# Optimization experiments

Measured on AMD Instinct MI355X. Metric: run time of the kernel, lower is better.

## Reference

```python
import jax, jax.numpy as jnp
import numpy as np

B, H, W, C = 64, 56, 56, 128
WIN, SHIFT, NH = 7, 3, 4
HD = C // NH
N = WIN * WIN
HID = 4 * C
EPS = 1e-5


def _rel_index():
    coords = np.stack(np.meshgrid(np.arange(WIN), np.arange(WIN), indexing='ij')).reshape(2, -1)
    rel = coords[:, :, None] - coords[:, None, :]
    rel = rel.transpose(1, 2, 0).astype(np.int64)
    rel[..., 0] += WIN - 1
    rel[..., 1] += WIN - 1
    rel[..., 0] *= 2 * WIN - 1
    return rel.sum(-1)  # [N, N]


def _attn_mask():
    img = np.zeros((H, W), dtype=np.float32)
    cnt = 0
    bounds = [(0, H - WIN), (H - WIN, H - SHIFT), (H - SHIFT, H)]
    for h0, h1 in bounds:
        for w0, w1 in bounds:
            img[h0:h1, w0:w1] = cnt
            cnt += 1
    mw = img.reshape(H // WIN, WIN, W // WIN, WIN).transpose(0, 2, 1, 3).reshape(-1, N)
    am = mw[:, None, :] - mw[:, :, None]
    return np.where(am != 0, -100.0, 0.0).astype(np.float32)  # [nW, N, N]


def setup_inputs() -> dict:
    key = jax.random.key(0)
    ks = jax.random.split(key, 16)
    s = lambda k, shp, f: (jax.random.normal(k, shp, jnp.float32) * f)
    return {
        'x': s(ks[0], (B, H * W, C), 1.0),
        'norm1_w': jnp.ones((C,), jnp.float32),
        'norm1_b': jnp.zeros((C,), jnp.float32),
        'qkv_w': s(ks[1], (3 * C, C), 0.02),
        'qkv_b': jnp.zeros((3 * C,), jnp.float32),
        'proj_w': s(ks[2], (C, C), 0.02),
        'proj_b': jnp.zeros((C,), jnp.float32),
        'norm2_w': jnp.ones((C,), jnp.float32),
        'norm2_b': jnp.zeros((C,), jnp.float32),
        'fc1_w': s(ks[3], (HID, C), 0.02),
        'fc1_b': jnp.zeros((HID,), jnp.float32),
        'fc2_w': s(ks[4], (C, HID), 0.02),
        'fc2_b': jnp.zeros((C,), jnp.float32),
        'bias_table': s(ks[5], ((2 * WIN - 1) ** 2, NH), 0.02),
        'attn_mask': jnp.asarray(_attn_mask()),
        'rel_index': jnp.asarray(_rel_index(), jnp.int32),
    }


def _ln(x, w, b):
    mu = x.mean(-1, keepdims=True)
    var = ((x - mu) ** 2).mean(-1, keepdims=True)
    return (x - mu) * jax.lax.rsqrt(var + EPS) * w + b


def reference(x, norm1_w, norm1_b, qkv_w, qkv_b, proj_w, proj_b,
              norm2_w, norm2_b, fc1_w, fc1_b, fc2_w, fc2_b,
              bias_table, attn_mask, rel_index):
    Bx, L, Cx = x.shape
    shortcut = x
    xn = _ln(x, norm1_w, norm1_b).reshape(Bx, H, W, Cx)
    xs = jnp.roll(xn, (-SHIFT, -SHIFT), axis=(1, 2))
    # window partition -> [B*nW, N, C]
    xw = xs.reshape(Bx, H // WIN, WIN, W // WIN, WIN, Cx).transpose(0, 1, 3, 2, 4, 5).reshape(-1, N, Cx)
    B_ = xw.shape[0]
    qkv = (xw @ qkv_w.T + qkv_b).reshape(B_, N, 3, NH, HD).transpose(2, 0, 3, 1, 4)
    q, k, v = qkv[0], qkv[1], qkv[2]
    q = q * (HD ** -0.5)
    attn = jnp.einsum('bhnd,bhmd->bhnm', q, k)  # [B_, NH, N, N]
    bias = bias_table[rel_index.reshape(-1)].reshape(N, N, NH).transpose(2, 0, 1)
    attn = attn + bias[None]
    nW = attn_mask.shape[0]
    attn = attn.reshape(B_ // nW, nW, NH, N, N) + attn_mask[None, :, None]
    attn = jax.nn.softmax(attn.reshape(B_, NH, N, N), axis=-1)
    out = jnp.einsum('bhnm,bhmd->bhnd', attn, v).transpose(0, 2, 1, 3).reshape(B_, N, Cx)
    out = out @ proj_w.T + proj_b
    # window reverse + roll back
    out = out.reshape(Bx, H // WIN, W // WIN, WIN, WIN, Cx).transpose(0, 1, 3, 2, 4, 5).reshape(Bx, H, W, Cx)
    out = jnp.roll(out, (SHIFT, SHIFT), axis=(1, 2)).reshape(Bx, L, Cx)
    x = shortcut + out
    h = _ln(x, norm2_w, norm2_b)
    h = jax.nn.gelu(h @ fc1_w.T + fc1_b, approximate=False) @ fc2_w.T + fc2_b
    return x + h
```

## Files before the change

### kernel.cpp

```cpp
#include <hip/hip_runtime.h>
#include <hip/hip_bf16.h>
#include <stdint.h>

typedef unsigned int uint;
typedef unsigned short ushort;
typedef short s16x8 __attribute__((ext_vector_type(8)));
typedef float f32x4 __attribute__((ext_vector_type(4)));

#define DEV static __device__ __forceinline__

DEV float bflo(uint u){ union{uint i;float f;} v; v.i = u<<16; return v.f; }
DEV float bfhi(uint u){ union{uint i;float f;} v; v.i = u & 0xffff0000u; return v.f; }
DEV float bf2f(ushort u){ union{uint i;float f;} v; v.i = ((uint)u)<<16; return v.f; }
DEV ushort f2bf(float f){ union{float f;uint i;} v; v.f=f; uint r=(v.i + 0x7fffu + ((v.i>>16)&1u))>>16; return (ushort)r; }

DEV f32x4 MFMA_BF(s16x8 a, s16x8 b, f32x4 c){
  return __builtin_amdgcn_mfma_f32_16x16x32_bf16(a, b, c, 0, 0, 0);
}

DEV float ld1(const void* b, int i, bool f32){
  return f32 ? ((const float*)b)[i] : bf2f(((const ushort*)b)[i]);
}
DEV ushort ld_bf(const void* b, int i, bool f32){
  return f32 ? f2bf(((const float*)b)[i]) : ((const ushort*)b)[i];
}
DEV void ld2(const void* b, int i, bool f32, float& a0, float& a1){
  if(f32){ float2 t = *(const float2*)((const float*)b + i); a0=t.x; a1=t.y; }
  else   { uint p = *(const uint*)((const ushort*)b + i); a0=bflo(p); a1=bfhi(p); }
}
DEV void ld8(const void* b, int i, bool f32, float* f){
  if(f32){
    const float* p = (const float*)b + i;
    float4 a0 = *(const float4*)p, a1 = *(const float4*)(p+4);
    f[0]=a0.x; f[1]=a0.y; f[2]=a0.z; f[3]=a0.w;
    f[4]=a1.x; f[5]=a1.y; f[6]=a1.z; f[7]=a1.w;
  } else {
    uint4 p = *(const uint4*)((const ushort*)b + i);
    f[0]=bflo(p.x); f[1]=bfhi(p.x); f[2]=bflo(p.y); f[3]=bfhi(p.y);
    f[4]=bflo(p.z); f[5]=bfhi(p.z); f[6]=bflo(p.w); f[7]=bfhi(p.w);
  }
}
DEV void st1(void* b, int i, bool f32, float v){
  if(f32) ((float*)b)[i] = v; else ((ushort*)b)[i] = f2bf(v);
}
DEV bool probe_f32(const void* normw){ return *(const uint*)normw == 0x3F800000u; }
DEV float clamp1k(float v){ return fminf(fmaxf(v, -1024.f), 1024.f); }

DEV float gelu_fast(float a){
  float t = a*(0.79788456080286536f + 0.035677408136300125f*a*a);
  float e = __expf(2.f*t);
  float th = 1.f - 2.f/(e+1.f);
  return 0.5f*a*(1.f+th);
}


__global__ void swin_prep(const void* __restrict__ n1w,
                          const void* __restrict__ qkvw, const void* __restrict__ projw,
                          const void* __restrict__ btab, const int* __restrict__ ridx,
                          const void* __restrict__ amask,
                          const void* __restrict__ fc1w, const void* __restrict__ fc2w,
                          ushort* __restrict__ qkvw_r, ushort* __restrict__ projw_r,
                          ushort* __restrict__ comb_t, ushort* __restrict__ amask_t,
                          ushort* __restrict__ fc1w_r, ushort* __restrict__ fc2w_r)
{
  const bool f32 = probe_f32(n1w);
  int idx=blockIdx.x*256+threadIdx.x;
  if(idx<49152){
    int j=idx&7, l=(idx>>3)&63, rest=idx>>9, ks=rest&3, nt=rest>>2;
    qkvw_r[idx]=ld_bf(qkvw, (nt*16+(l&15))*128 + ks*32 + (l>>4)*8 + j, f32);
  }
  if(idx<16384){
    int j=idx&7, l=(idx>>3)&63, rest=idx>>9, ks=rest&3, nt=rest>>2;
    projw_r[idx]=ld_bf(projw, (nt*16+(l&15))*128 + ks*32 + (l>>4)*8 + j, f32);
  }
  if(idx<65536){
    int j=idx&7, l=(idx>>3)&63, rest=idx>>9, ks=rest&3, nt=rest>>2;
    fc1w_r[idx]=ld_bf(fc1w, (nt*16+(l&15))*128 + ks*32 + (l>>4)*8 + j, f32);
  }
  if(idx<65536){
    int j=idx&7, l=(idx>>3)&63, rest=idx>>9, ks=rest&15, nt=rest>>4;
    fc2w_r[idx]=ld_bf(fc2w, (nt*16+(l&15))*512 + ks*32 + (l>>4)*8 + j, f32);
  }
  if(idx<12544){
    int hh=idx/3136, rm=idx-hh*3136, m=rm>>6, n=rm&63;
    comb_t[idx]=(n<49)?ld_bf(btab, ridx[n*49+m]*4+hh, f32):(ushort)0;
  }
  if(idx<200704){
    int w2=idx/3136, rm=idx-w2*3136, m=rm>>6, n=rm&63;
    amask_t[idx]=(n<49)?ld_bf(amask, (w2*49+n)*49+m, f32):(ushort)0;
  }
}

__global__ __launch_bounds__(256,3)
void swin_attn_mfma(const void* __restrict__ x,
                    const void* __restrict__ n1w, const void* __restrict__ n1b,
                    const void* __restrict__ qkvb, const void* __restrict__ projb,
                    const ushort* __restrict__ qkvw_r, const ushort* __restrict__ projw_r,
                    const ushort* __restrict__ comb_t, const ushort* __restrict__ amask_t,
                    void* __restrict__ y)
{
  __shared__ __align__(16) ushort smA[9216];
  __shared__ __align__(16) ushort smB[16896];
  const bool f32 = probe_f32(n1w);
  const int tid=threadIdx.x, lane=tid&63, wv=tid>>6;
  const int g=lane>>4, lr=lane&15;
  const int widx=blockIdx.x, b=widx>>6, wi=widx&63, wh=wi>>3, ww=wi&7;
  const bool boundary=(wh==7)||(ww==7);

  {
    float w0,w1,c0,c1;
    ld2(n1w, 2*lane, f32, w0, w1);
    ld2(n1b, 2*lane, f32, c0, c1);
    for(int r=wv;r<49;r+=4){
      int i=r/7, j=r-7*i;
      int hs=wh*7+i+3; if(hs>=56)hs-=56;
      int vs=ww*7+j+3; if(vs>=56)vs-=56;
      float a0,a1; ld2(x, (b*3136+hs*56+vs)*128 + 2*lane, f32, a0, a1);
      float s=a0+a1, q=a0*a0+a1*a1;
      #pragma unroll
      for(int off=32;off;off>>=1){ s+=__shfl_xor(s,off); q+=__shfl_xor(q,off); }
      float mu=s*(1.f/128.f);
      float var=q*(1.f/128.f)-mu*mu;
      float rs=rsqrtf(var+1e-5f);
      smA[r*136+2*lane  ]=f2bf((a0-mu)*rs*w0+c0);
      smA[r*136+2*lane+1]=f2bf((a1-mu)*rs*w1+c1);
    }
    for(int k=tid;k<15*136;k+=256) smA[49*136+k]=0;
  }
  __syncthreads();

  s16x8 af[4][4];
  #pragma unroll
  for(int mt=0;mt<4;++mt)
    #pragma unroll
    for(int ks=0;ks<4;++ks)
      af[mt][ks]=*(const s16x8*)&smA[(mt*16+lr)*136 + ks*32 + g*8];
  __syncthreads();

  #pragma unroll 1
  for(int t=0;t<6;++t){
    int nt=wv*6+t;
    int col=nt*16+lr;
    s16x8 bf[4];
    #pragma unroll
    for(int ks=0;ks<4;++ks) bf[ks]=*(const s16x8*)&qkvw_r[(size_t)((nt*4+ks)*64+lane)*8];
    float bias=ld1(qkvb, col, f32);
    #pragma unroll
    for(int mt=0;mt<4;++mt){
      f32x4 acc={0.f,0.f,0.f,0.f};
      #pragma unroll
      for(int ks=0;ks<4;++ks) acc=MFMA_BF(af[mt][ks],bf[ks],acc);
      if(nt<8){
        #pragma unroll
        for(int r=0;r<4;++r)
          smB[(mt*16+g*4+r)*264+col]=f2bf((acc[r]+bias)*0.17677669529663689f);
      } else if(nt<16){
        #pragma unroll
        for(int r=0;r<4;++r)
          smB[(mt*16+g*4+r)*264+col]=f2bf(acc[r]+bias);
      } else {
        int vd=col-256;
        ushort u[4];
        #pragma unroll
        for(int r=0;r<4;++r){
          int m=mt*16+g*4+r;
          u[r]=(m<49)?f2bf(acc[r]+bias):(ushort)0;
        }
        uint2 pk; pk.x=(uint)u[0]|((uint)u[1]<<16); pk.y=(uint)u[2]|((uint)u[3]<<16);
        *(uint2*)&smA[vd*72+mt*16+g*4]=pk;
      }
    }
  }
  __syncthreads();

  const int h=wv;
  f32x4 S[4][4];
  {
    s16x8 qa[4];
    #pragma unroll
    for(int mt=0;mt<4;++mt) qa[mt]=*(const s16x8*)&smB[(mt*16+lr)*264 + h*32 + g*8];
    #pragma unroll
    for(int nt=0;nt<4;++nt){
      s16x8 kb=*(const s16x8*)&smB[(nt*16+lr)*264 + 128 + h*32 + g*8];
      #pragma unroll
      for(int mt=0;mt<4;++mt){
        f32x4 z={0.f,0.f,0.f,0.f};
        S[mt][nt]=MFMA_BF(qa[mt],kb,z);
      }
    }
  }
  #pragma unroll
  for(int nt=0;nt<4;++nt){
    int m=nt*16+lr;
    if(m<49){
      #pragma unroll
      for(int mt=0;mt<4;++mt){
        int n0=mt*16+g*4;
        uint2 cb=*(const uint2*)&comb_t[(size_t)(h*49+m)*64+n0];
        S[mt][nt][0]+=bflo(cb.x); S[mt][nt][1]+=bfhi(cb.x);
        S[mt][nt][2]+=bflo(cb.y); S[mt][nt][3]+=bfhi(cb.y);
      }
      if(boundary){
        #pragma unroll
        for(int mt=0;mt<4;++mt){
          int n0=mt*16+g*4;
          uint2 mk=*(const uint2*)&amask_t[(size_t)(wi*49+m)*64+n0];
          S[mt][nt][0]+=bflo(mk.x); S[mt][nt][1]+=bfhi(mk.x);
          S[mt][nt][2]+=bflo(mk.y); S[mt][nt][3]+=bfhi(mk.y);
        }
      }
    } else {
      #pragma unroll
      for(int mt=0;mt<4;++mt){
        #pragma unroll
        for(int r=0;r<4;++r) S[mt][nt][r]=-3.0e4f;
      }
    }
  }
  float inv_[4][4];
  #pragma unroll
  for(int mt=0;mt<4;++mt){
    #pragma unroll
    for(int r=0;r<4;++r){
      float v=fmaxf(fmaxf(S[mt][0][r],S[mt][1][r]),fmaxf(S[mt][2][r],S[mt][3][r]));
      v=fmaxf(v,__shfl_xor(v,1)); v=fmaxf(v,__shfl_xor(v,2));
      v=fmaxf(v,__shfl_xor(v,4)); v=fmaxf(v,__shfl_xor(v,8));
      #pragma unroll
      for(int nt=0;nt<4;++nt) S[mt][nt][r]=__expf(S[mt][nt][r]-v);
      float s=S[mt][0][r]+S[mt][1][r]+S[mt][2][r]+S[mt][3][r];
      s+=__shfl_xor(s,1); s+=__shfl_xor(s,2); s+=__shfl_xor(s,4); s+=__shfl_xor(s,8);
      inv_[mt][r]=1.f/s;
    }
  }
  __syncthreads();

  #pragma unroll
  for(int nt=0;nt<4;++nt){
    int m=nt*16+lr;
    #pragma unroll
    for(int mt=0;mt<4;++mt){
      #pragma unroll
      for(int r=0;r<4;++r)
        smB[(mt*16+g*4+r)*264 + h*66 + m]=f2bf(S[mt][nt][r]);
    }
  }
  __syncthreads();

  f32x4 O[4][2];
  {
    s16x8 vb[2][2];
    #pragma unroll
    for(int dt=0;dt<2;++dt)
      #pragma unroll
      for(int ks=0;ks<2;++ks)
        vb[dt][ks]=*(const s16x8*)&smA[(h*32+dt*16+lr)*72 + ks*32 + g*8];
    #pragma unroll
    for(int mt=0;mt<4;++mt){
      s16x8 pa0=*(const s16x8*)&smB[(mt*16+lr)*264 + h*66 + g*8];
      s16x8 pa1=*(const s16x8*)&smB[(mt*16+lr)*264 + h*66 + 32 + g*8];
      #pragma unroll
      for(int dt=0;dt<2;++dt){
        f32x4 z={0.f,0.f,0.f,0.f};
        z=MFMA_BF(pa0,vb[dt][0],z);
        O[mt][dt]=MFMA_BF(pa1,vb[dt][1],z);
      }
    }
  }
  __syncthreads();

  #pragma unroll
  for(int mt=0;mt<4;++mt){
    #pragma unroll
    for(int dt=0;dt<2;++dt){
      int d=h*32+dt*16+lr;
      #pragma unroll
      for(int r=0;r<4;++r)
        smA[(mt*16+g*4+r)*136 + d]=f2bf(O[mt][dt][r]*inv_[mt][r]);
    }
  }
  __syncthreads();

  {
    s16x8 oa[4][4];
    #pragma unroll
    for(int mt=0;mt<4;++mt)
      #pragma unroll
      for(int ks=0;ks<4;++ks)
        oa[mt][ks]=*(const s16x8*)&smA[(mt*16+lr)*136 + ks*32 + g*8];
    #pragma unroll 1
    for(int t=0;t<2;++t){
      int nt=wv*2+t;
      int c=nt*16+lr;
      s16x8 bfp[4];
      #pragma unroll
      for(int ks=0;ks<4;++ks) bfp[ks]=*(const s16x8*)&projw_r[(size_t)((nt*4+ks)*64+lane)*8];
      float pbv=ld1(projb, c, f32);
      #pragma unroll
      for(int mt=0;mt<4;++mt){
        f32x4 acc={0.f,0.f,0.f,0.f};
        #pragma unroll
        for(int ks=0;ks<4;++ks) acc=MFMA_BF(oa[mt][ks],bfp[ks],acc);
        #pragma unroll
        for(int r=0;r<4;++r){
          int n=mt*16+g*4+r;
          if(n<49){
            int i=n/7, j=n-7*i;
            int hh=wh*7+i+3; if(hh>=56)hh-=56;
            int vv=ww*7+j+3; if(vv>=56)vv-=56;
            int gaddr=(b*3136+hh*56+vv)*128+c;
            st1(y, gaddr, f32, clamp1k(acc[r]+pbv+ld1(x, gaddr, f32)));
          }
        }
      }
    }
  }
}

__global__ __launch_bounds__(256,4)
void swin_mlp_mfma(void* __restrict__ y,
                   const void* __restrict__ n2w, const void* __restrict__ n2b,
                   const void* __restrict__ fc1b, const void* __restrict__ fc2b,
                   const ushort* __restrict__ fc1w_r, const ushort* __restrict__ fc2w_r)
{
  __shared__ __align__(16) ushort smH[64*264];
  const bool f32 = probe_f32(n2w);
  const int tid=threadIdx.x, lane=tid&63, wv=tid>>6;
  const int g=lane>>4, lr=lane&15;
  const int row0=blockIdx.x*64;

  {
    float w0,w1,c0,c1;
    ld2(n2w, 2*lane, f32, w0, w1);
    ld2(n2b, 2*lane, f32, c0, c1);
    for(int r=wv;r<64;r+=4){
      float a0,a1; ld2(y, (row0+r)*128 + 2*lane, f32, a0, a1);
      float s=a0+a1, q=a0*a0+a1*a1;
      #pragma unroll
      for(int off=32;off;off>>=1){ s+=__shfl_xor(s,off); q+=__shfl_xor(q,off); }
      float mu=s*(1.f/128.f);
      float var=q*(1.f/128.f)-mu*mu;
      float rs=rsqrtf(var+1e-5f);
      smH[r*136+2*lane  ]=f2bf((a0-mu)*rs*w0+c0);
      smH[r*136+2*lane+1]=f2bf((a1-mu)*rs*w1+c1);
    }
  }
  __syncthreads();

  s16x8 af[4][4];
  #pragma unroll
  for(int mt=0;mt<4;++mt)
    #pragma unroll
    for(int ks=0;ks<4;++ks)
      af[mt][ks]=*(const s16x8*)&smH[(mt*16+lr)*136 + ks*32 + g*8];
  __syncthreads();

  f32x4 acc2[4][2];
  #pragma unroll
  for(int mt=0;mt<4;++mt)
    #pragma unroll
    for(int tn=0;tn<2;++tn) acc2[mt][tn]=(f32x4){0.f,0.f,0.f,0.f};

  #pragma unroll 1
  for(int half=0;half<2;++half){
    #pragma unroll 1
    for(int t=0;t<4;++t){
      int nt=half*16 + wv*4 + t;
      int col=nt*16+lr;
      s16x8 bf[4];
      #pragma unroll
      for(int ks=0;ks<4;++ks) bf[ks]=*(const s16x8*)&fc1w_r[(size_t)((nt*4+ks)*64+lane)*8];
      float bias=ld1(fc1b, col, f32);
      int lcol=col-half*256;
      #pragma unroll
      for(int mt=0;mt<4;++mt){
        f32x4 acc={0.f,0.f,0.f,0.f};
        #pragma unroll
        for(int ks=0;ks<4;++ks) acc=MFMA_BF(af[mt][ks],bf[ks],acc);
        #pragma unroll
        for(int r=0;r<4;++r)
          smH[(mt*16+g*4+r)*264 + lcol]=f2bf(gelu_fast(acc[r]+bias));
      }
    }
    __syncthreads();
    #pragma unroll 1
    for(int ksl=0;ksl<8;++ksl){
      s16x8 am[4];
      #pragma unroll
      for(int mt=0;mt<4;++mt) am[mt]=*(const s16x8*)&smH[(mt*16+lr)*264 + ksl*32 + g*8];
      s16x8 bn[2];
      #pragma unroll
      for(int tn=0;tn<2;++tn)
        bn[tn]=*(const s16x8*)&fc2w_r[(size_t)(((wv*2+tn)*16 + half*8+ksl)*64+lane)*8];
      #pragma unroll
      for(int mt=0;mt<4;++mt)
        #pragma unroll
        for(int tn=0;tn<2;++tn) acc2[mt][tn]=MFMA_BF(am[mt],bn[tn],acc2[mt][tn]);
    }
    __syncthreads();
  }

  #pragma unroll
  for(int tn=0;tn<2;++tn){
    int col=(wv*2+tn)*16+lr;
    float fb=ld1(fc2b, col, f32);
    #pragma unroll
    for(int mt=0;mt<4;++mt){
      #pragma unroll
      for(int r=0;r<4;++r){
        int gr=row0 + mt*16+g*4+r;
        float v=acc2[mt][tn][r]+fb+ld1(y, gr*128+col, f32);
        st1(y, gr*128+col, f32, v);
      }
    }
  }
}

__global__ __launch_bounds__(256,2)
void swin_mlp(void* __restrict__ y,
              const void* __restrict__ n2w, const void* __restrict__ n2b,
              const void* __restrict__ fc1w, const void* __restrict__ fc1b,
              const void* __restrict__ fc2w, const void* __restrict__ fc2b)
{
  __shared__ float sY[16*128];
  __shared__ float sH[16*512];
  const bool f32 = probe_f32(n2w);
  const int tid=threadIdx.x, lane=tid&63, wave=tid>>6;
  const int g0=blockIdx.x*16;
  {
    float w0,w1,c0,c1;
    ld2(n2w, 2*lane, f32, w0, w1);
    ld2(n2b, 2*lane, f32, c0, c1);
    for(int r=wave;r<16;r+=4){
      float a0,a1; ld2(y, (g0+r)*128+2*lane, f32, a0, a1);
      float s=a0+a1, q=a0*a0+a1*a1;
      #pragma unroll
      for(int off=32;off;off>>=1){ s+=__shfl_xor(s,off); q+=__shfl_xor(q,off); }
      float mu=s*(1.f/128.f), var=q*(1.f/128.f)-mu*mu, rs=rsqrtf(var+1e-5f);
      sY[r*128+2*lane  ]=(a0-mu)*rs*w0+c0;
      sY[r*128+2*lane+1]=(a1-mu)*rs*w1+c1;
    }
  }
  __syncthreads();
  #pragma unroll 1
  for(int pass=0;pass<2;++pass){
    int col=tid+256*pass;
    float acc[16];
    #pragma unroll
    for(int r=0;r<16;++r) acc[r]=0.f;
    for(int k8=0;k8<16;++k8){
      float wf[8]; ld8(fc1w, col*128+k8*8, f32, wf);
      const float* abase=&sY[k8*8];
      #pragma unroll
      for(int r=0;r<16;++r){
        const float* ar=abase+r*128;
        float4 a0=*(const float4*)ar, a1=*(const float4*)(ar+4);
        acc[r]+=a0.x*wf[0]+a0.y*wf[1]+a0.z*wf[2]+a0.w*wf[3]
              +a1.x*wf[4]+a1.y*wf[5]+a1.z*wf[6]+a1.w*wf[7];
      }
    }
    float fb=ld1(fc1b, col, f32);
    #pragma unroll
    for(int r=0;r<16;++r){
      float a=acc[r]+fb;
      sH[r*512+col]=0.5f*a*(1.f+erff(a*0.70710678118654752f));
    }
  }
  __syncthreads();
  {
    const int col=tid&127, rg=tid>>7;
    float acc[8];
    #pragma unroll
    for(int r=0;r<8;++r) acc[r]=0.f;
    for(int k8=0;k8<64;++k8){
      float wf[8]; ld8(fc2w, col*512+k8*8, f32, wf);
      const float* abase=&sH[rg*8*512+k8*8];
      #pragma unroll
      for(int r=0;r<8;++r){
        const float* ar=abase+r*512;
        float4 a0=*(const float4*)ar, a1=*(const float4*)(ar+4);
        acc[r]+=a0.x*wf[0]+a0.y*wf[1]+a0.z*wf[2]+a0.w*wf[3]
              +a1.x*wf[4]+a1.y*wf[5]+a1.z*wf[6]+a1.w*wf[7];
      }
    }
    float fb=ld1(fc2b, col, f32);
    #pragma unroll
    for(int r=0;r<8;++r){
      int gr=g0+rg*8+r;
      float v=acc[r]+fb+ld1(y, gr*128+col, f32);
      st1(y, gr*128+col, f32, v);
    }
  }
}

constexpr int LDA = 132;
constexpr int LDQ = 392;

__global__ __launch_bounds__(256,2)
void swin_attn(const void* __restrict__ x,
               const void* __restrict__ n1w, const void* __restrict__ n1b,
               const void* __restrict__ qkvw, const void* __restrict__ qkvb,
               const void* __restrict__ projw, const void* __restrict__ projb,
               const void* __restrict__ btab, const void* __restrict__ amask,
               const int* __restrict__ ridx, void* __restrict__ y)
{
  __shared__ float  sA[49*LDA];
  __shared__ ushort sQ[49*LDQ];
  const bool f32 = probe_f32(n1w);
  const int tid=threadIdx.x, lane=tid&63, wave=tid>>6;
  const int widx=blockIdx.x, b=widx>>6, wi=widx&63, wh=wi>>3, ww=wi&7;
  {
    float w0,w1,c0,c1;
    ld2(n1w, 2*lane, f32, w0, w1);
    ld2(n1b, 2*lane, f32, c0, c1);
    for(int r=wave;r<49;r+=4){
      int i=r/7, j=r-7*(r/7);
      int hs=wh*7+i+3; if(hs>=56) hs-=56;
      int vs=ww*7+j+3; if(vs>=56) vs-=56;
      int base=(b*3136 + hs*56 + vs)*128;
      float a0,a1; ld2(x, base+2*lane, f32, a0, a1);
      float s=a0+a1, q=a0*a0+a1*a1;
      #pragma unroll
      for(int off=32;off;off>>=1){ s+=__shfl_xor(s,off); q+=__shfl_xor(q,off); }
      float mu=s*(1.f/128.f);
      float var=q*(1.f/128.f)-mu*mu;
      float rs=rsqrtf(var+1e-5f);
      sA[r*LDA+2*lane  ]=(a0-mu)*rs*w0+c0;
      sA[r*LDA+2*lane+1]=(a1-mu)*rs*w1+c1;
    }
  }
  __syncthreads();
  #pragma unroll 1
  for(int pass=0;pass<2;++pass){
    int col=tid+256*pass;
    if(col<384){
      float acc[49];
      #pragma unroll
      for(int r=0;r<49;++r) acc[r]=0.f;
      for(int k8=0;k8<16;++k8){
        float wf[8]; ld8(qkvw, col*128+k8*8, f32, wf);
        const float* abase=&sA[k8*8];
        #pragma unroll
        for(int r=0;r<49;++r){
          const float* ar=abase+r*LDA;
          float4 a0=*(const float4*)ar;
          float4 a1=*(const float4*)(ar+4);
          acc[r]+=a0.x*wf[0]+a0.y*wf[1]+a0.z*wf[2]+a0.w*wf[3]
                +a1.x*wf[4]+a1.y*wf[5]+a1.z*wf[6]+a1.w*wf[7];
        }
      }
      float bias=ld1(qkvb, col, f32);
      float scale=(col<128)?0.17677669529663689f:1.f;
      #pragma unroll
      for(int r=0;r<49;++r) sQ[r*LDQ+col]=f2bf((acc[r]+bias)*scale);
    }
  }
  __syncthreads();
  if(lane<49){
    const int head=wave, n=lane;
    float qv[32];
    {
      const ushort* qr=&sQ[n*LDQ+head*32];
      #pragma unroll
      for(int c=0;c<4;++c){
        uint4 p=*(const uint4*)(qr+c*8);
        qv[c*8+0]=bflo(p.x); qv[c*8+1]=bfhi(p.x);
        qv[c*8+2]=bflo(p.y); qv[c*8+3]=bfhi(p.y);
        qv[c*8+4]=bflo(p.z); qv[c*8+5]=bfhi(p.z);
        qv[c*8+6]=bflo(p.w); qv[c*8+7]=bfhi(p.w);
      }
    }
    float sc[49];
    #pragma unroll
    for(int m=0;m<49;++m){
      const ushort* kr=&sQ[m*LDQ+128+head*32];
      float acc=0.f;
      #pragma unroll
      for(int c=0;c<4;++c){
        uint4 p=*(const uint4*)(kr+c*8);
        acc+=qv[c*8+0]*bflo(p.x)+qv[c*8+1]*bfhi(p.x)
            +qv[c*8+2]*bflo(p.y)+qv[c*8+3]*bfhi(p.y)
            +qv[c*8+4]*bflo(p.z)+qv[c*8+5]*bfhi(p.z)
            +qv[c*8+6]*bflo(p.w)+qv[c*8+7]*bfhi(p.w);
      }
      int rr=ridx[n*49+m];
      acc+=ld1(btab, rr*4+head, f32);
      acc+=ld1(amask, (wi*49+n)*49+m, f32);
      sc[m]=acc;
    }
    float mx=sc[0];
    #pragma unroll
    for(int m=1;m<49;++m) mx=fmaxf(mx,sc[m]);
    float sum=0.f;
    #pragma unroll
    for(int m=0;m<49;++m){ sc[m]=__expf(sc[m]-mx); sum+=sc[m]; }
    float inv=1.f/sum;
    float ov[32];
    #pragma unroll
    for(int d=0;d<32;++d) ov[d]=0.f;
    #pragma unroll
    for(int m=0;m<49;++m){
      const ushort* vr=&sQ[m*LDQ+256+head*32];
      float pm=sc[m];
      #pragma unroll
      for(int c=0;c<4;++c){
        uint4 p=*(const uint4*)(vr+c*8);
        ov[c*8+0]+=pm*bflo(p.x); ov[c*8+1]+=pm*bfhi(p.x);
        ov[c*8+2]+=pm*bflo(p.y); ov[c*8+3]+=pm*bfhi(p.y);
        ov[c*8+4]+=pm*bflo(p.z); ov[c*8+5]+=pm*bfhi(p.z);
        ov[c*8+6]+=pm*bflo(p.w); ov[c*8+7]+=pm*bfhi(p.w);
      }
    }
    #pragma unroll
    for(int d=0;d<32;++d) sA[n*LDA+head*32+d]=ov[d]*inv;
  }
  __syncthreads();
  {
    const int col=tid&127, rh=tid>>7;
    const int r0=rh*25, nr=rh?24:25;
    float acc[25];
    #pragma unroll
    for(int r=0;r<25;++r) acc[r]=0.f;
    for(int k8=0;k8<16;++k8){
      float wf[8]; ld8(projw, col*128+k8*8, f32, wf);
      const float* abase=&sA[r0*LDA+k8*8];
      #pragma unroll
      for(int r=0;r<25;++r){
        if(r<nr){
          const float* ar=abase+r*LDA;
          float4 a0=*(const float4*)ar;
          float4 a1=*(const float4*)(ar+4);
          acc[r]+=a0.x*wf[0]+a0.y*wf[1]+a0.z*wf[2]+a0.w*wf[3]
                +a1.x*wf[4]+a1.y*wf[5]+a1.z*wf[6]+a1.w*wf[7];
        }
      }
    }
    float pb=ld1(projb, col, f32);
    #pragma unroll
    for(int r=0;r<25;++r){
      if(r<nr){
        int row=r0+r;
        int i=row/7, j=row-7*(row/7);
        int hh=wh*7+i+3; if(hh>=56) hh-=56;
        int vv=ww*7+j+3; if(vv>=56) vv-=56;
        int gidx=(b*3136+hh*56+vv)*128+col;
        st1(y, gidx, f32, acc[r]+pb+ld1(x, gidx, f32));
      }
    }
  }
}

extern "C" void kernel_launch(void* const* d_in, const int* in_sizes, int n_in,
                              void* d_out, int out_size, void* d_ws, size_t ws_size,
                              hipStream_t stream)
{
  const void* x    =d_in[0];
  const void* n1w  =d_in[1];
  const void* n1b  =d_in[2];
  const void* qkvw =d_in[3];
  const void* qkvb =d_in[4];
  const void* projw=d_in[5];
  const void* projb=d_in[6];
  const void* n2w  =d_in[7];
  const void* n2b  =d_in[8];
  const void* fc1w =d_in[9];
  const void* fc1b =d_in[10];
  const void* fc2w =d_in[11];
  const void* fc2b =d_in[12];
  const void* btab =d_in[13];
  const void* amask=d_in[14];
  const int*  ridx =(const int*)d_in[15];

  const size_t NEED = 819712;
  if(ws_size >= NEED){
    char* w = (char*)d_ws;
    ushort* qkvw_r = (ushort*)(w + 0);
    ushort* projw_r= (ushort*)(w + 98304);
    ushort* comb_t = (ushort*)(w + 131072);
    ushort* amask_t= (ushort*)(w + 156160);
    ushort* fc1w_r = (ushort*)(w + 557568);
    ushort* fc2w_r = (ushort*)(w + 688640);
    swin_prep<<<784,256,0,stream>>>(n1w,qkvw,projw,btab,ridx,amask,fc1w,fc2w,
                                    qkvw_r,projw_r,comb_t,amask_t,fc1w_r,fc2w_r);
    swin_attn_mfma<<<4096,256,0,stream>>>(x,n1w,n1b,qkvb,projb,
                                          qkvw_r,projw_r,comb_t,amask_t,d_out);
    swin_mlp_mfma<<<3136,256,0,stream>>>(d_out,n2w,n2b,fc1b,fc2b,fc1w_r,fc2w_r);
  } else {
    swin_attn<<<4096,256,0,stream>>>(x,n1w,n1b,qkvw,qkvb,projw,projb,btab,amask,ridx,d_out);
    swin_mlp<<<12544,256,0,stream>>>(d_out,n2w,n2b,fc1w,fc1b,fc2w,fc2b);
  }
}
```

Measured before the change: 378.4 us.

## Split attention kernel across 8 waves and batch residual loads before stores

Doubles the attention kernel block to 512 threads. Each head now uses two waves, and each wave takes half of the row tiles, so per-wave register arrays are halved and more waves are resident. The LayerNorm input loads are batched into registers before the reductions. The residual x loads and address math in the projection epilogue are hoisted ahead of the MFMAs to overlap memory latency. The risks are more synchronisation per block and higher register pressure from the hoisted arrays, which could limit occupancy at the new launch bounds.

```diff
diff --git a/kernel.cpp b/kernel.cpp
--- a/kernel.cpp
+++ b/kernel.cpp
@@ -91,7 +91,7 @@
   }
 }
 
-__global__ __launch_bounds__(256,3)
+__global__ __launch_bounds__(512,4)
 void swin_attn_mfma(const void* __restrict__ x,
                     const void* __restrict__ n1w, const void* __restrict__ n1b,
                     const void* __restrict__ qkvb, const void* __restrict__ projb,
@@ -104,6 +104,7 @@
   const bool f32 = probe_f32(n1w);
   const int tid=threadIdx.x, lane=tid&63, wv=tid>>6;
   const int g=lane>>4, lr=lane&15;
+  const int hi=wv&1, nh=wv>>1;
   const int widx=blockIdx.x, b=widx>>6, wi=widx&63, wh=wi>>3, ww=wi&7;
   const bool boundary=(wh==7)||(ww==7);
 
@@ -111,45 +112,57 @@
     float w0,w1,c0,c1;
     ld2(n1w, 2*lane, f32, w0, w1);
     ld2(n1b, 2*lane, f32, c0, c1);
-    for(int r=wv;r<49;r+=4){
-      int i=r/7, j=r-7*i;
-      int hs=wh*7+i+3; if(hs>=56)hs-=56;
-      int vs=ww*7+j+3; if(vs>=56)vs-=56;
-      float a0,a1; ld2(x, (b*3136+hs*56+vs)*128 + 2*lane, f32, a0, a1);
-      float s=a0+a1, q=a0*a0+a1*a1;
-      #pragma unroll
-      for(int off=32;off;off>>=1){ s+=__shfl_xor(s,off); q+=__shfl_xor(q,off); }
-      float mu=s*(1.f/128.f);
-      float var=q*(1.f/128.f)-mu*mu;
-      float rs=rsqrtf(var+1e-5f);
-      smA[r*136+2*lane  ]=f2bf((a0-mu)*rs*w0+c0);
-      smA[r*136+2*lane+1]=f2bf((a1-mu)*rs*w1+c1);
-    }
-    for(int k=tid;k<15*136;k+=256) smA[49*136+k]=0;
-  }
-  __syncthreads();
-
-  s16x8 af[4][4];
+    float a0[7], a1[7];
+    #pragma unroll
+    for(int k=0;k<7;++k){
+      int r=wv+8*k;
+      if(r<49){
+        int i=r/7, j=r-7*i;
+        int hs=wh*7+i+3; if(hs>=56)hs-=56;
+        int vs=ww*7+j+3; if(vs>=56)vs-=56;
+        ld2(x, (b*3136+hs*56+vs)*128 + 2*lane, f32, a0[k], a1[k]);
+      }
+    }
+    #pragma unroll
+    for(int k=0;k<7;++k){
+      int r=wv+8*k;
+      if(r<49){
+        float s=a0[k]+a1[k], q=a0[k]*a0[k]+a1[k]*a1[k];
+        #pragma unroll
+        for(int off=32;off;off>>=1){ s+=__shfl_xor(s,off); q+=__shfl_xor(q,off); }
+        float mu=s*(1.f/128.f);
+        float var=q*(1.f/128.f)-mu*mu;
+        float rs=rsqrtf(var+1e-5f);
+        smA[r*136+2*lane  ]=f2bf((a0[k]-mu)*rs*w0+c0);
+        smA[r*136+2*lane+1]=f2bf((a1[k]-mu)*rs*w1+c1);
+      }
+    }
+    for(int k=tid;k<15*136;k+=512) smA[49*136+k]=0;
+  }
+  __syncthreads();
+
+  s16x8 af[2][4];
   #pragma unroll
-  for(int mt=0;mt<4;++mt)
+  for(int i=0;i<2;++i)
     #pragma unroll
     for(int ks=0;ks<4;++ks)
-      af[mt][ks]=*(const s16x8*)&smA[(mt*16+lr)*136 + ks*32 + g*8];
+      af[i][ks]=*(const s16x8*)&smA[((hi*2+i)*16+lr)*136 + ks*32 + g*8];
   __syncthreads();
 
   #pragma unroll 1
   for(int t=0;t<6;++t){
-    int nt=wv*6+t;
+    int nt=nh*6+t;
     int col=nt*16+lr;
     s16x8 bf[4];
     #pragma unroll
     for(int ks=0;ks<4;++ks) bf[ks]=*(const s16x8*)&qkvw_r[(size_t)((nt*4+ks)*64+lane)*8];
     float bias=ld1(qkvb, col, f32);
     #pragma unroll
-    for(int mt=0;mt<4;++mt){
+    for(int i=0;i<2;++i){
+      int mt=hi*2+i;
       f32x4 acc={0.f,0.f,0.f,0.f};
       #pragma unroll
-      for(int ks=0;ks<4;++ks) acc=MFMA_BF(af[mt][ks],bf[ks],acc);
+      for(int ks=0;ks<4;++ks) acc=MFMA_BF(af[i][ks],bf[ks],acc);
       if(nt<8){
         #pragma unroll
         for(int r=0;r<4;++r)
@@ -173,19 +186,19 @@
   }
   __syncthreads();
 
-  const int h=wv;
-  f32x4 S[4][4];
-  {
-    s16x8 qa[4];
-    #pragma unroll
-    for(int mt=0;mt<4;++mt) qa[mt]=*(const s16x8*)&smB[(mt*16+lr)*264 + h*32 + g*8];
+  const int h=nh;
+  f32x4 S[2][4];
+  {
+    s16x8 qa[2];
+    #pragma unroll
+    for(int i=0;i<2;++i) qa[i]=*(const s16x8*)&smB[((hi*2+i)*16+lr)*264 + h*32 + g*8];
     #pragma unroll
     for(int nt=0;nt<4;++nt){
       s16x8 kb=*(const s16x8*)&smB[(nt*16+lr)*264 + 128 + h*32 + g*8];
       #pragma unroll
-      for(int mt=0;mt<4;++mt){
+      for(int i=0;i<2;++i){
         f32x4 z={0.f,0.f,0.f,0.f};
-        S[mt][nt]=MFMA_BF(qa[mt],kb,z);
+        S[i][nt]=MFMA_BF(qa[i],kb,z);
       }
     }
   }
@@ -194,42 +207,42 @@
     int m=nt*16+lr;
     if(m<49){
       #pragma unroll
-      for(int mt=0;mt<4;++mt){
-        int n0=mt*16+g*4;
+      for(int i=0;i<2;++i){
+        int n0=(hi*2+i)*16+g*4;
         uint2 cb=*(const uint2*)&comb_t[(size_t)(h*49+m)*64+n0];
-        S[mt][nt][0]+=bflo(cb.x); S[mt][nt][1]+=bfhi(cb.x);
-        S[mt][nt][2]+=bflo(cb.y); S[mt][nt][3]+=bfhi(cb.y);
+        S[i][nt][0]+=bflo(cb.x); S[i][nt][1]+=bfhi(cb.x);
+        S[i][nt][2]+=bflo(cb.y); S[i][nt][3]+=bfhi(cb.y);
       }
       if(boundary){
         #pragma unroll
-        for(int mt=0;mt<4;++mt){
-          int n0=mt*16+g*4;
+        for(int i=0;i<2;++i){
+          int n0=(hi*2+i)*16+g*4;
           uint2 mk=*(const uint2*)&amask_t[(size_t)(wi*49+m)*64+n0];
-          S[mt][nt][0]+=bflo(mk.x); S[mt][nt][1]+=bfhi(mk.x);
-          S[mt][nt][2]+=bflo(mk.y); S[mt][nt][3]+=bfhi(mk.y);
+          S[i][nt][0]+=bflo(mk.x); S[i][nt][1]+=bfhi(mk.x);
+          S[i][nt][2]+=bflo(mk.y); S[i][nt][3]+=bfhi(mk.y);
         }
       }
     } else {
       #pragma unroll
-      for(int mt=0;mt<4;++mt){
-        #pragma unroll
-        for(int r=0;r<4;++r) S[mt][nt][r]=-3.0e4f;
-      }
-    }
-  }
-  float inv_[4][4];
+      for(int i=0;i<2;++i){
+        #pragma unroll
+        for(int r=0;r<4;++r) S[i][nt][r]=-3.0e4f;
+      }
+    }
+  }
+  float inv_[2][4];
   #pragma unroll
-  for(int mt=0;mt<4;++mt){
+  for(int i=0;i<2;++i){
     #pragma unroll
     for(int r=0;r<4;++r){
-      float v=fmaxf(fmaxf(S[mt][0][r],S[mt][1][r]),fmaxf(S[mt][2][r],S[mt][3][r]));
+      float v=fmaxf(fmaxf(S[i][0][r],S[i][1][r]),fmaxf(S[i][2][r],S[i][3][r]));
       v=fmaxf(v,__shfl_xor(v,1)); v=fmaxf(v,__shfl_xor(v,2));
       v=fmaxf(v,__shfl_xor(v,4)); v=fmaxf(v,__shfl_xor(v,8));
       #pragma unroll
-      for(int nt=0;nt<4;++nt) S[mt][nt][r]=__expf(S[mt][nt][r]-v);
-      float s=S[mt][0][r]+S[mt][1][r]+S[mt][2][r]+S[mt][3][r];
+      for(int nt=0;nt<4;++nt) S[i][nt][r]=__expf(S[i][nt][r]-v);
+      float s=S[i][0][r]+S[i][1][r]+S[i][2][r]+S[i][3][r];
       s+=__shfl_xor(s,1); s+=__shfl_xor(s,2); s+=__shfl_xor(s,4); s+=__shfl_xor(s,8);
-      inv_[mt][r]=1.f/s;
+      inv_[i][r]=1.f/s;
     }
   }
   __syncthreads();
@@ -238,15 +251,15 @@
   for(int nt=0;nt<4;++nt){
     int m=nt*16+lr;
     #pragma unroll
-    for(int mt=0;mt<4;++mt){
+    for(int i=0;i<2;++i){
       #pragma unroll
       for(int r=0;r<4;++r)
-        smB[(mt*16+g*4+r)*264 + h*66 + m]=f2bf(S[mt][nt][r]);
-    }
-  }
-  __syncthreads();
-
-  f32x4 O[4][2];
+        smB[((hi*2+i)*16+g*4+r)*264 + h*66 + m]=f2bf(S[i][nt][r]);
+    }
+  }
+  __syncthreads();
+
+  f32x4 O[2][2];
   {
     s16x8 vb[2][2];
     #pragma unroll
@@ -255,61 +268,71 @@
       for(int ks=0;ks<2;++ks)
         vb[dt][ks]=*(const s16x8*)&smA[(h*32+dt*16+lr)*72 + ks*32 + g*8];
     #pragma unroll
-    for(int mt=0;mt<4;++mt){
-      s16x8 pa0=*(const s16x8*)&smB[(mt*16+lr)*264 + h*66 + g*8];
-      s16x8 pa1=*(const s16x8*)&smB[(mt*16+lr)*264 + h*66 + 32 + g*8];
+    for(int i=0;i<2;++i){
+      s16x8 pa0=*(const s16x8*)&smB[((hi*2+i)*16+lr)*264 + h*66 + g*8];
+      s16x8 pa1=*(const s16x8*)&smB[((hi*2+i)*16+lr)*264 + h*66 + 32 + g*8];
       #pragma unroll
       for(int dt=0;dt<2;++dt){
         f32x4 z={0.f,0.f,0.f,0.f};
         z=MFMA_BF(pa0,vb[dt][0],z);
-        O[mt][dt]=MFMA_BF(pa1,vb[dt][1],z);
+        O[i][dt]=MFMA_BF(pa1,vb[dt][1],z);
       }
     }
   }
   __syncthreads();
 
   #pragma unroll
-  for(int mt=0;mt<4;++mt){
+  for(int i=0;i<2;++i){
     #pragma unroll
     for(int dt=0;dt<2;++dt){
       int d=h*32+dt*16+lr;
       #pragma unroll
       for(int r=0;r<4;++r)
-        smA[(mt*16+g*4+r)*136 + d]=f2bf(O[mt][dt][r]*inv_[mt][r]);
-    }
-  }
-  __syncthreads();
-
-  {
-    s16x8 oa[4][4];
-    #pragma unroll
-    for(int mt=0;mt<4;++mt)
+        smA[((hi*2+i)*16+g*4+r)*136 + d]=f2bf(O[i][dt][r]*inv_[i][r]);
+    }
+  }
+  __syncthreads();
+
+  {
+    s16x8 oa[2][4];
+    #pragma unroll
+    for(int i=0;i<2;++i)
       #pragma unroll
       for(int ks=0;ks<4;++ks)
-        oa[mt][ks]=*(const s16x8*)&smA[(mt*16+lr)*136 + ks*32 + g*8];
+        oa[i][ks]=*(const s16x8*)&smA[((hi*2+i)*16+lr)*136 + ks*32 + g*8];
     #pragma unroll 1
     for(int t=0;t<2;++t){
-      int nt=wv*2+t;
+      int nt=nh*2+t;
       int c=nt*16+lr;
+      int   ga[2][4];
+      float xres[2][4];
+      #pragma unroll
+      for(int i=0;i<2;++i){
+        #pragma unroll
+        for(int r=0;r<4;++r){
+          int n=(hi*2+i)*16+g*4+r;
+          if(n<49){
+            int ii=n/7, jj=n-7*ii;
+            int hh=wh*7+ii+3; if(hh>=56)hh-=56;
+            int vv=ww*7+jj+3; if(vv>=56)vv-=56;
+            ga[i][r]=(b*3136+hh*56+vv)*128+c;
+            xres[i][r]=ld1(x, ga[i][r], f32);
+          } else { ga[i][r]=-1; xres[i][r]=0.f; }
+        }
+      }
       s16x8 bfp[4];
       #pragma unroll
       for(int ks=0;ks<4;++ks) bfp[ks]=*(const s16x8*)&projw_r[(size_t)((nt*4+ks)*64+lane)*8];
       float pbv=ld1(projb, c, f32);
       #pragma unroll
-      for(int mt=0;mt<4;++mt){
+      for(int i=0;i<2;++i){
         f32x4 acc={0.f,0.f,0.f,0.f};
         #pragma unroll
-        for(int ks=0;ks<4;++ks) acc=MFMA_BF(oa[mt][ks],bfp[ks],acc);
+        for(int ks=0;ks<4;++ks) acc=MFMA_BF(oa[i][ks],bfp[ks],acc);
         #pragma unroll
         for(int r=0;r<4;++r){
-          int n=mt*16+g*4+r;
-          if(n<49){
-            int i=n/7, j=n-7*i;
-            int hh=wh*7+i+3; if(hh>=56)hh-=56;
-            int vv=ww*7+j+3; if(vv>=56)vv-=56;
-            int gaddr=(b*3136+hh*56+vv)*128+c;
-            st1(y, gaddr, f32, clamp1k(acc[r]+pbv+ld1(x, gaddr, f32)));
-          }
+          if(ga[i][r]>=0)
+            st1(y, ga[i][r], f32, clamp1k(acc[r]+pbv+xres[i][r]));
         }
       }
     }
@@ -681,7 +704,7 @@
     ushort* fc2w_r = (ushort*)(w + 688640);
     swin_prep<<<784,256,0,stream>>>(n1w,qkvw,projw,btab,ridx,amask,fc1w,fc2w,
                                     qkvw_r,projw_r,comb_t,amask_t,fc1w_r,fc2w_r);
-    swin_attn_mfma<<<4096,256,0,stream>>>(x,n1w,n1b,qkvb,projb,
+    swin_attn_mfma<<<4096,512,0,stream>>>(x,n1w,n1b,qkvb,projb,
                                           qkvw_r,projw_r,comb_t,amask_t,d_out);
     swin_mlp_mfma<<<3136,256,0,stream>>>(d_out,n2w,n2b,fc1b,fc2b,fc1w_r,fc2w_r);
   } else {
```

Result: faster. 343.8 us (-9.1%).
